# Kernel optimization log

Hardware: AMD Instinct MI355X
Metric: run time of the kernel (lower is better)

The kernel has to match this reference:

```python
import jax, jax.numpy as jnp
import numpy as np

V, D, L, H, S, B = 32000, 512, 4, 8, 2048, 2
HD = D // H
FF = 4 * D
EPS = 1e-5


def _ln(x, w, b):
    m = jnp.mean(x, axis=-1, keepdims=True)
    v = jnp.var(x, axis=-1, keepdims=True)
    return (x - m) / jnp.sqrt(v + EPS) * w + b


def setup_inputs() -> dict:
    key = jax.random.key(0)
    ks = jax.random.split(key, 32)
    rn = lambda k, shape, s=0.02: jax.random.normal(k, shape, jnp.float32) * s
    return {
        'x': jax.random.randint(ks[0], (B, S), 0, V),
        'tok_emb': rn(ks[1], (V, D)),
        'pos_emb': rn(ks[2], (S, D)),
        'qw': rn(ks[3], (L, D, D)), 'qb': rn(ks[4], (L, D)),
        'kw': rn(ks[5], (L, D, D)), 'kb': rn(ks[6], (L, D)),
        'vw': rn(ks[7], (L, D, D)), 'vb': rn(ks[8], (L, D)),
        'ow': rn(ks[9], (L, D, D)), 'ob': rn(ks[10], (L, D)),
        'qphase': rn(ks[11], (L, H), 0.1),
        'sp_phase': rn(ks[12], (L, D), 0.1),
        'n1w': jnp.ones((L, D), jnp.float32), 'n1b': jnp.zeros((L, D), jnp.float32),
        'n2w': jnp.ones((L, D), jnp.float32), 'n2b': jnp.zeros((L, D), jnp.float32),
        'f1w': rn(ks[13], (L, D, FF)), 'f1b': rn(ks[14], (L, FF)),
        'f2w': rn(ks[15], (L, FF, D)), 'f2b': rn(ks[16], (L, D)),
        'iw': rn(ks[17], (L, D, D)), 'ib': rn(ks[18], (L, D)),
        'gw': rn(ks[19], (L, D, D)), 'gb': rn(ks[20], (L, D)),
        'nw': jnp.ones((D,), jnp.float32), 'nb': jnp.zeros((D,), jnp.float32),
        'outw': rn(ks[21], (D, V)), 'outb': rn(ks[22], (V,)),
    }


def _forward(x, tok_emb, pos_emb, qw, qb, kw, kb, vw, vb, ow, ob, qphase, sp_phase,
             n1w, n1b, n2w, n2b, f1w, f1b, f2w, f2b, iw, ib, gw, gb, nw, nb, outw, outb):
    Bx, Sx = x.shape
    h = tok_emb[x] + pos_emb[:Sx][None, :, :]          # [B,S,D]
    mask = jnp.tril(jnp.ones((Sx, Sx), dtype=bool))    # causal
    scale = 1.0 / np.sqrt(HD).astype(np.float32)
    for l in range(L):
        # quantum attention with phase-modulated scores
        hn = _ln(h, n1w[l], n1b[l])
        q = (hn @ qw[l] + qb[l]).reshape(Bx, Sx, H, HD)
        k = (hn @ kw[l] + kb[l]).reshape(Bx, Sx, H, HD)
        v = (hn @ vw[l] + vb[l]).reshape(Bx, Sx, H, HD)
        scores = jnp.einsum('bqhd,bkhd->bhqk', q, k) * scale
        qi = jnp.cos(qphase[l][None, :, None, None] * scores)
        scores = scores * (1.0 + 0.1 * qi)
        scores = jnp.where(mask[None, None], scores, -jnp.inf)
        attn = jax.nn.softmax(scores, axis=-1)
        o = jnp.einsum('bhqk,bkhd->bqhd', attn, v).reshape(Bx, Sx, D)
        h = h + o @ ow[l] + ob[l]
        # superposition: x * cos(phase * x)
        h = h * jnp.cos(sp_phase[l] * h)
        # feed-forward (exact GELU, as torch default)
        hn2 = _ln(h, n2w[l], n2b[l])
        h = h + jax.nn.gelu(hn2 @ f1w[l] + f1b[l], approximate=False) @ f2w[l] + f2b[l]
        # interference gate
        g = jax.nn.sigmoid(h @ gw[l] + gb[l])
        h = (h @ iw[l] + ib[l]) * g + h * (1.0 - g)
    h = _ln(h, nw, nb)
    return h @ outw + outb                              # [B,S,V] logits


def reference(x, tok_emb, pos_emb, qw, qb, kw, kb, vw, vb, ow, ob, qphase, sp_phase,
              n1w, n1b, n2w, n2b, f1w, f1b, f2w, f2b, iw, ib, gw, gb, nw, nb, outw, outb):
    return _forward(x, tok_emb, pos_emb, qw, qb, kw, kb, vw, vb, ow, ob, qphase, sp_phase,
                    n1w, n1b, n2w, n2b, f1w, f1b, f2w, f2b, iw, ib, gw, gb, nw, nb, outw, outb)
```

## Files before the change

kernel.cpp:

```cpp
#include <hip/hip_runtime.h>
#include <math.h>

#define DIM 512
#define NH 8
#define HD 64
#define SEQ 2048
#define BATCH 2
#define NLAYER 4
#define FFD 2048
#define VOCAB 32000
#define ROWS (BATCH*SEQ)
#define QKV_LD 1536

typedef unsigned short u16;
typedef __attribute__((ext_vector_type(8))) short bfrag;
typedef __attribute__((ext_vector_type(4))) short sfrag4;
typedef __attribute__((ext_vector_type(4))) float facc;

__device__ __forceinline__ u16 f2bf(float f){
  unsigned u = __builtin_bit_cast(unsigned, f);
  u += 0x7fff + ((u>>16)&1);
  return (u16)(u>>16);
}

typedef __attribute__((address_space(3))) unsigned int lds_u32;
typedef const __attribute__((address_space(1))) unsigned int glob_u32;
__device__ __forceinline__ void gload16(const void* g, void* l){
  __builtin_amdgcn_global_load_lds((glob_u32*)g, (lds_u32*)l, 16, 0, 0);
}

template<int N> __device__ __forceinline__ void wait_vmcnt(){
  if constexpr (N==0)      asm volatile("s_waitcnt vmcnt(0)" ::: "memory");
  else if constexpr (N==3) asm volatile("s_waitcnt vmcnt(3)" ::: "memory");
  else if constexpr (N==4) asm volatile("s_waitcnt vmcnt(4)" ::: "memory");
  else if constexpr (N==6) asm volatile("s_waitcnt vmcnt(6)" ::: "memory");
  else if constexpr (N==8) asm volatile("s_waitcnt vmcnt(8)" ::: "memory");
  else static_assert(N==0, "unsupported vmcnt");
}

__global__ void transpose_w(const float* __restrict__ in, u16* __restrict__ out,
                            int K, int N, size_t zStride, int nOff, int imode){
  __shared__ float t[32][33];
  const int bz = blockIdx.z;
  const float* I = in + (size_t)bz*K*N;
  u16* O = out + (size_t)bz*zStride;
  const int n0 = blockIdx.x*32, k0 = blockIdx.y*32;
  #pragma unroll
  for (int i=0;i<4;i++){
    int k = k0 + threadIdx.y + 8*i;
    t[threadIdx.y+8*i][threadIdx.x] = I[(size_t)k*N + n0 + threadIdx.x];
  }
  __syncthreads();
  #pragma unroll
  for (int i=0;i<4;i++){
    int n = n0 + threadIdx.y + 8*i;
    int np = (imode==0) ? n : ((n>>4)*32 + (n&15) + (imode==2 ? 16 : 0));
    O[(size_t)(nOff+np)*K + k0 + threadIdx.x] = f2bf(t[threadIdx.x][threadIdx.y+8*i]);
  }
}

__global__ void concat3_k(const float* __restrict__ a, const float* __restrict__ b,
                          const float* __restrict__ c, float* __restrict__ o){
  int idx = blockIdx.x*256 + threadIdx.x;
  int l = idx/1536, r = idx%1536;
  float v = (r<512) ? a[l*512+r] : (r<1024 ? b[l*512+r-512] : c[l*512+r-1024]);
  o[idx] = v;
}
__global__ void concat2i_k(const float* __restrict__ ib, const float* __restrict__ gb,
                           float* __restrict__ o){
  int idx = blockIdx.x*256 + threadIdx.x;
  int l = idx>>10, cp = idx&1023;
  int bb = cp>>4, c = (bb>>1)*16 + (cp&15);
  o[idx] = (bb&1) ? gb[l*512+c] : ib[l*512+c];
}

__global__ void embed_k(const int* __restrict__ x, const float* __restrict__ tok,
                        const float* __restrict__ pos, float* __restrict__ h){
  int idx = blockIdx.x*256 + threadIdx.x;
  int row = idx >> 7;
  int d4  = idx & 127;
  int s   = row & (SEQ-1);
  int tkn = x[row];
  float4 tv = *(const float4*)(tok + (size_t)tkn*DIM + d4*4);
  float4 pv = *(const float4*)(pos + (size_t)s*DIM + d4*4);
  float4 r; r.x=tv.x+pv.x; r.y=tv.y+pv.y; r.z=tv.z+pv.z; r.w=tv.w+pv.w;
  *(float4*)(h + (size_t)row*DIM + d4*4) = r;
}

__global__ __launch_bounds__(256) void ln_k(const float* __restrict__ h,
    const float* __restrict__ w, const float* __restrict__ bsc,
    u16* __restrict__ out){
  const int wid = threadIdx.x>>6, lane = threadIdx.x&63;
  const int row = blockIdx.x*4 + wid;
  const float* r = h + (size_t)row*DIM + lane*8;
  float4 v0 = *(const float4*)r;
  float4 v1 = *(const float4*)(r+4);
  float s  = v0.x+v0.y+v0.z+v0.w + v1.x+v1.y+v1.z+v1.w;
  float ss = v0.x*v0.x+v0.y*v0.y+v0.z*v0.z+v0.w*v0.w
           + v1.x*v1.x+v1.y*v1.y+v1.z*v1.z+v1.w*v1.w;
  #pragma unroll
  for (int m=1;m<64;m<<=1){ s += __shfl_xor(s,m); ss += __shfl_xor(ss,m); }
  const float mean = s*(1.f/DIM);
  const float var  = ss*(1.f/DIM) - mean*mean;
  const float rsd  = rsqrtf(var + 1e-5f);
  float4 w0 = *(const float4*)(w + lane*8);
  float4 w1 = *(const float4*)(w + lane*8 + 4);
  float4 b0 = *(const float4*)(bsc + lane*8);
  float4 b1 = *(const float4*)(bsc + lane*8 + 4);
  bfrag pk;
  pk[0]=(short)f2bf((v0.x-mean)*rsd*w0.x+b0.x);
  pk[1]=(short)f2bf((v0.y-mean)*rsd*w0.y+b0.y);
  pk[2]=(short)f2bf((v0.z-mean)*rsd*w0.z+b0.z);
  pk[3]=(short)f2bf((v0.w-mean)*rsd*w0.w+b0.w);
  pk[4]=(short)f2bf((v1.x-mean)*rsd*w1.x+b1.x);
  pk[5]=(short)f2bf((v1.y-mean)*rsd*w1.y+b1.y);
  pk[6]=(short)f2bf((v1.z-mean)*rsd*w1.z+b1.z);
  pk[7]=(short)f2bf((v1.w-mean)*rsd*w1.w+b1.w);
  *(bfrag*)&out[(size_t)row*DIM + lane*8] = pk;
}

template<int BM,int BN,int BK,int WRN,int WCN,int DEPTH,int MODE>
__global__ __launch_bounds__(WRN*WCN*64, 2) void gemm_p(
    const u16* __restrict__ A, const u16* __restrict__ BT,
    const float* __restrict__ bias, const float* __restrict__ aux,
    float* __restrict__ Cf, u16* __restrict__ Cb, u16* __restrict__ vt,
    int M, int N, int K){
  constexpr int NTH = WRN*WCN*64;
  constexpr int FI  = BM/(16*WRN);
  constexpr int FJ  = BN/(16*WCN);
  constexpr int CPR = BK/8;
  constexpr int LA  = BM*CPR/NTH;
  constexpr int LB  = BN*CPR/NTH;
  constexpr int LPT = LA+LB;
  constexpr int NKK = BK/32;
  extern __shared__ __align__(16) u16 smem[];
  u16* lds_a = smem;
  u16* lds_b = smem + DEPTH*BM*BK;

  const int tid = threadIdx.x;
  const int wid = tid>>6, lane = tid&63;
  const int wr = wid / WCN, wc = wid % WCN;
  const int lr = lane&15, lg = lane>>4;
  const unsigned nwg = gridDim.x*gridDim.y;
  const unsigned lin = blockIdx.y*gridDim.x + blockIdx.x;
  const unsigned q = nwg >> 3;
  const unsigned sw = (lin & 7)*q + (lin >> 3);
  const int tm = sw % gridDim.x, tn = sw / gridDim.x;

  auto swzf = [](int row)->int{ return (BK==64) ? (row&7) : ((row>>1)&3); };

  auto stage = [&](int t, int buf){
    const int k0 = t*BK;
    #pragma unroll
    for (int i=0;i<LA;i++){
      int u = i*NTH + tid;
      int row = u/CPR, c = (u%CPR) ^ swzf(row);
      gload16(&A[(size_t)(tm*BM+row)*K + k0 + c*8], &lds_a[buf*BM*BK + u*8]);
    }
    #pragma unroll
    for (int i=0;i<LB;i++){
      int u = i*NTH + tid;
      int row = u/CPR, c = (u%CPR) ^ swzf(row);
      gload16(&BT[(size_t)(tn*BN+row)*K + k0 + c*8], &lds_b[buf*BN*BK + u*8]);
    }
  };

  facc acc[FI][FJ] = {};
  const int NT = K/BK;
  stage(0,0);
  if (NT>1) stage(1,1);
  if constexpr (DEPTH==3) { if (NT>2) stage(2,2); }
  for (int t=0;t<NT;t++){
    const int buf = t % DEPTH;
    const u16* la = &lds_a[buf*BM*BK];
    const u16* lb = &lds_b[buf*BN*BK];
    const int rem = NT-1-t;
    if constexpr (DEPTH==3){
      if (rem >= 2) wait_vmcnt<2*LPT>();
      else if (rem == 1) wait_vmcnt<LPT>();
      else wait_vmcnt<0>();
    } else {
      if (rem >= 1) wait_vmcnt<LPT>(); else wait_vmcnt<0>();
    }
    __builtin_amdgcn_s_barrier();
    __builtin_amdgcn_sched_barrier(0);
    bfrag af[FI], bf[FJ];
    #pragma unroll
    for (int i=0;i<FI;i++){
      int row = wr*(FI*16) + i*16 + lr;
      af[i] = *(const bfrag*)&la[row*BK + ((lg ^ swzf(row))*8)];
    }
    #pragma unroll
    for (int j=0;j<FJ;j++){
      int row = wc*(FJ*16) + j*16 + lr;
      bf[j] = *(const bfrag*)&lb[row*BK + ((lg ^ swzf(row))*8)];
    }
    if constexpr (NKK==1){
      asm volatile("s_waitcnt lgkmcnt(0)" ::: "memory");
      __builtin_amdgcn_sched_barrier(0);
      __builtin_amdgcn_s_barrier();
      __builtin_amdgcn_sched_barrier(0);
      if (t+DEPTH<NT) stage(t+DEPTH, buf);
      __builtin_amdgcn_s_setprio(1);
      #pragma unroll
      for (int i=0;i<FI;i++)
        #pragma unroll
        for (int j=0;j<FJ;j++)
          acc[i][j] = __builtin_amdgcn_mfma_f32_16x16x32_bf16(af[i], bf[j], acc[i][j],0,0,0);
      __builtin_amdgcn_s_setprio(0);
    } else {
      __builtin_amdgcn_s_setprio(1);
      #pragma unroll
      for (int i=0;i<FI;i++)
        #pragma unroll
        for (int j=0;j<FJ;j++)
          acc[i][j] = __builtin_amdgcn_mfma_f32_16x16x32_bf16(af[i], bf[j], acc[i][j],0,0,0);
      __builtin_amdgcn_s_setprio(0);
      bfrag af1[FI], bf1[FJ];
      #pragma unroll
      for (int i=0;i<FI;i++){
        int row = wr*(FI*16) + i*16 + lr;
        af1[i] = *(const bfrag*)&la[row*BK + (((4+lg) ^ swzf(row))*8)];
      }
      #pragma unroll
      for (int j=0;j<FJ;j++){
        int row = wc*(FJ*16) + j*16 + lr;
        bf1[j] = *(const bfrag*)&lb[row*BK + (((4+lg) ^ swzf(row))*8)];
      }
      asm volatile("s_waitcnt lgkmcnt(0)" ::: "memory");
      __builtin_amdgcn_sched_barrier(0);
      __builtin_amdgcn_s_barrier();
      __builtin_amdgcn_sched_barrier(0);
      if (t+DEPTH<NT) stage(t+DEPTH, buf);
      __builtin_amdgcn_s_setprio(1);
      #pragma unroll
      for (int i=0;i<FI;i++)
        #pragma unroll
        for (int j=0;j<FJ;j++)
          acc[i][j] = __builtin_amdgcn_mfma_f32_16x16x32_bf16(af1[i], bf1[j], acc[i][j],0,0,0);
      __builtin_amdgcn_s_setprio(0);
    }
  }

  if constexpr (MODE==5){
    #pragma unroll
    for (int i=0;i<FI;i++){
      #pragma unroll
      for (int j=0;j<FJ;j+=2){
        const int colp = tn*BN + wc*(FJ*16) + j*16;
        const int c = (colp>>5)*16 + lr;
        const float bi = bias[colp + lr];
        const float bg = bias[colp + 16 + lr];
        #pragma unroll
        for (int r=0;r<4;r++){
          const int row = tm*BM + wr*(FI*16) + i*16 + lg*4 + r;
          float vi = acc[i][j][r]   + bi;
          float vg = acc[i][j+1][r] + bg;
          float g  = 1.f/(1.f+__expf(-vg));
          const size_t o = (size_t)row*DIM + c;
          float hv = Cf[o];
          Cf[o] = vi*g + hv*(1.f-g);
        }
      }
    }
  } else if constexpr (MODE==7){
    #pragma unroll
    for (int i=0;i<FI;i++){
      #pragma unroll
      for (int j=0;j<FJ;j++){
        const int colblk = tn*BN + wc*(FJ*16) + j*16;
        const float bv = bias[colblk + lr];
        if (colblk < 1024){
          #pragma unroll
          for (int r=0;r<4;r++){
            const int row = tm*BM + wr*(FI*16) + i*16 + lg*4 + r;
            Cb[(size_t)row*N + colblk + lr] = f2bf(acc[i][j][r] + bv);
          }
        } else {
          const int c = colblk + lr - 1024;
          const int hh = c>>6, d = c&63;
          const int row0 = tm*BM + wr*(FI*16) + i*16 + lg*4;
          const int b = row0>>11, s0 = row0&2047;
          sfrag4 pk;
          #pragma unroll
          for (int r=0;r<4;r++) pk[r] = (short)f2bf(acc[i][j][r] + bv);
          *(sfrag4*)&vt[((size_t)((b*NH+hh)*HD + d))*SEQ + s0] = pk;
        }
      }
    }
  } else {
    #pragma unroll
    for (int i=0;i<FI;i++){
      #pragma unroll
      for (int j=0;j<FJ;j++){
        const int col = tn*BN + wc*(FJ*16) + j*16 + lr;
        const float bv = bias ? bias[col] : 0.f;
        #pragma unroll
        for (int r=0;r<4;r++){
          const int row = tm*BM + wr*(FI*16) + i*16 + lg*4 + r;
          float v = acc[i][j][r] + bv;
          const size_t o = (size_t)row*N + col;
          if      (MODE==0) Cf[o] = v;
          else if (MODE==3){ float g = 0.5f*v*(1.f+erff(v*0.70710678118f)); Cb[o] = f2bf(g); }
          else if (MODE==4){ float t = Cf[o] + v; t = t*__cosf(aux[col]*t); Cf[o] = t; }
          else if (MODE==6){ float t = Cf[o] + v; Cf[o] = t; Cb[o] = f2bf(t); }
        }
      }
    }
  }
}

__global__ __launch_bounds__(256) void attn_k(
    const u16* __restrict__ QKV, const u16* __restrict__ VT,
    const float* __restrict__ qphase, u16* __restrict__ O){
  __shared__ __align__(16) u16 lds_p[4][16*64];
  const int bx = blockIdx.x;
  const int qblk = (bx&1) ? (31 - (bx>>1)) : (bx>>1);
  const int hh = blockIdx.y, b = blockIdx.z;
  const int tid = threadIdx.x;
  const int wid = tid>>6, lane = tid&63;
  const int lr = lane&15, lg = lane>>4;
  const int qbase = qblk*64 + wid*16;
  const float ph = qphase[hh];
  const float scale = 0.125f;
  u16* pbuf = lds_p[wid];

  bfrag aq[2];
  #pragma unroll
  for (int st=0; st<2; st++)
    aq[st] = *(const bfrag*)&QKV[(size_t)(b*SEQ + qbase + lr)*QKV_LD + hh*HD + st*32 + lg*8];

  facc oacc[4] = {};
  float lrow[4] = {0.f,0.f,0.f,0.f};

  const int nkv = qblk + 1;
  for (int kt=0; kt<nkv; kt++){
    const int kv0 = kt*64;
    facc sc[4];
    #pragma unroll
    for (int j=0;j<4;j++){
      bfrag bk0 = *(const bfrag*)&QKV[(size_t)(b*SEQ + kv0 + j*16 + lr)*QKV_LD + 512 + hh*HD + lg*8];
      bfrag bk1 = *(const bfrag*)&QKV[(size_t)(b*SEQ + kv0 + j*16 + lr)*QKV_LD + 512 + hh*HD + 32 + lg*8];
      facc z = (facc){0.f,0.f,0.f,0.f};
      z     = __builtin_amdgcn_mfma_f32_16x16x32_bf16(aq[0], bk0, z, 0,0,0);
      sc[j] = __builtin_amdgcn_mfma_f32_16x16x32_bf16(aq[1], bk1, z, 0,0,0);
    }
    float pv[4][4];
    #pragma unroll
    for (int j=0;j<4;j++)
      #pragma unroll
      for (int r=0;r<4;r++){
        int srow = qbase + lg*4 + r;
        int scol = kv0 + j*16 + lr;
        float xv = sc[j][r]*scale;
        xv = xv*(1.f + 0.1f*__cosf(ph*xv));
        if (scol > srow) xv = -1e30f;
        pv[j][r] = __expf(xv);
      }
    #pragma unroll
    for (int r=0;r<4;r++){
      float rs = (pv[0][r]+pv[1][r]) + (pv[2][r]+pv[3][r]);
      rs += __shfl_xor(rs,1);
      rs += __shfl_xor(rs,2);
      rs += __shfl_xor(rs,4);
      rs += __shfl_xor(rs,8);
      lrow[r] += rs;
    }
    #pragma unroll
    for (int j=0;j<4;j++)
      #pragma unroll
      for (int r=0;r<4;r++){
        int prow = lg*4 + r;
        pbuf[prow*64 + ((j*16+lr) ^ ((prow&7)<<3))] = f2bf(pv[j][r]);
      }
    #pragma unroll
    for (int ks=0; ks<2; ks++){
      bfrag pa = *(const bfrag*)&pbuf[lr*64 + ((ks*32 + lg*8) ^ ((lr&7)<<3))];
      #pragma unroll
      for (int n=0;n<4;n++){
        bfrag vb = *(const bfrag*)&VT[((size_t)((b*NH + hh)*HD + n*16 + lr))*SEQ + kv0 + ks*32 + lg*8];
        oacc[n] = __builtin_amdgcn_mfma_f32_16x16x32_bf16(pa, vb, oacc[n], 0,0,0);
      }
    }
  }
  float rcp[4];
  #pragma unroll
  for (int r=0;r<4;r++) rcp[r] = 1.f/lrow[r];
  #pragma unroll
  for (int n=0;n<4;n++)
    #pragma unroll
    for (int r=0;r<4;r++){
      float val = oacc[n][r] * rcp[r];
      O[(size_t)(b*SEQ + qbase + lg*4 + r)*DIM + hh*HD + n*16 + lr] = f2bf(val);
    }
}

extern "C" void kernel_launch(void* const* d_in, const int* in_sizes, int n_in,
                              void* d_out, int out_size, void* d_ws, size_t ws_size,
                              hipStream_t stream){
  const int*   x        = (const int*)d_in[0];
  const float* tok_emb  = (const float*)d_in[1];
  const float* pos_emb  = (const float*)d_in[2];
  const float* qw = (const float*)d_in[3];  const float* qb = (const float*)d_in[4];
  const float* kw = (const float*)d_in[5];  const float* kb = (const float*)d_in[6];
  const float* vw = (const float*)d_in[7];  const float* vb = (const float*)d_in[8];
  const float* ow = (const float*)d_in[9];  const float* ob = (const float*)d_in[10];
  const float* qphase   = (const float*)d_in[11];
  const float* sp_phase = (const float*)d_in[12];
  const float* n1w = (const float*)d_in[13]; const float* n1b = (const float*)d_in[14];
  const float* n2w = (const float*)d_in[15]; const float* n2b = (const float*)d_in[16];
  const float* f1w = (const float*)d_in[17]; const float* f1b = (const float*)d_in[18];
  const float* f2w = (const float*)d_in[19]; const float* f2b = (const float*)d_in[20];
  const float* iw  = (const float*)d_in[21]; const float* ib  = (const float*)d_in[22];
  const float* gw  = (const float*)d_in[23]; const float* gb  = (const float*)d_in[24];
  const float* nw  = (const float*)d_in[25]; const float* nb  = (const float*)d_in[26];
  const float* outw= (const float*)d_in[27]; const float* outb= (const float*)d_in[28];
  float* out = (float*)d_out;

  char* base = (char*)d_ws;
  size_t off = 0;
  auto alloc = [&](size_t bytes)->void*{
    void* p = base + off; off += bytes; off = (off + 255) & ~(size_t)255; return p;
  };
  float* h    = (float*)alloc((size_t)ROWS*DIM*4);
  u16* hn     = (u16*)alloc((size_t)ROWS*DIM*2);
  u16* qkvB   = (u16*)alloc((size_t)ROWS*QKV_LD*2);
  u16* vTb    = (u16*)alloc((size_t)ROWS*DIM*2);
  u16* oB     = (u16*)alloc((size_t)ROWS*DIM*2);
  u16* hB     = (u16*)alloc((size_t)ROWS*DIM*2);
  u16* ffB    = (u16*)alloc((size_t)ROWS*FFD*2);
  u16* qkvT = (u16*)alloc((size_t)NLAYER*1536*DIM*2);
  u16* owT  = (u16*)alloc((size_t)NLAYER*DIM*DIM*2);
  u16* igT  = (u16*)alloc((size_t)NLAYER*1024*DIM*2);
  u16* f1T  = (u16*)alloc((size_t)NLAYER*DIM*FFD*2);
  u16* f2T  = (u16*)alloc((size_t)NLAYER*DIM*FFD*2);
  u16* outT = (u16*)alloc((size_t)VOCAB*DIM*2);
  float* qkvb = (float*)alloc((size_t)NLAYER*1536*4);
  float* igb  = (float*)alloc((size_t)NLAYER*1024*4);

  dim3 tb(32,8);
  transpose_w<<<dim3(DIM/32, DIM/32, NLAYER), tb, 0, stream>>>(qw, qkvT, DIM, DIM, (size_t)1536*DIM, 0, 0);
  transpose_w<<<dim3(DIM/32, DIM/32, NLAYER), tb, 0, stream>>>(kw, qkvT, DIM, DIM, (size_t)1536*DIM, 512, 0);
  transpose_w<<<dim3(DIM/32, DIM/32, NLAYER), tb, 0, stream>>>(vw, qkvT, DIM, DIM, (size_t)1536*DIM, 1024, 0);
  transpose_w<<<dim3(DIM/32, DIM/32, NLAYER), tb, 0, stream>>>(ow, owT, DIM, DIM, (size_t)DIM*DIM, 0, 0);
  transpose_w<<<dim3(DIM/32, DIM/32, NLAYER), tb, 0, stream>>>(iw, igT, DIM, DIM, (size_t)1024*DIM, 0, 1);
  transpose_w<<<dim3(DIM/32, DIM/32, NLAYER), tb, 0, stream>>>(gw, igT, DIM, DIM, (size_t)1024*DIM, 0, 2);
  transpose_w<<<dim3(FFD/32, DIM/32, NLAYER), tb, 0, stream>>>(f1w, f1T, DIM, FFD, (size_t)DIM*FFD, 0, 0);
  transpose_w<<<dim3(DIM/32, FFD/32, NLAYER), tb, 0, stream>>>(f2w, f2T, FFD, DIM, (size_t)DIM*FFD, 0, 0);
  transpose_w<<<dim3(VOCAB/32, DIM/32, 1),    tb, 0, stream>>>(outw, outT, DIM, VOCAB, 0, 0, 0);
  concat3_k<<<NLAYER*1536/256, 256, 0, stream>>>(qb, kb, vb, qkvb);
  concat2i_k<<<NLAYER*1024/256, 256, 0, stream>>>(ib, gb, igb);

  embed_k<<<ROWS*DIM/4/256, 256, 0, stream>>>(x, tok_emb, pos_emb, h);

  constexpr size_t SM_MID = 3*(128+128)*32*2;
  constexpr size_t SM_ROW = 3*(64+128)*32*2;
  constexpr size_t SM_BIG = 2*(256+256)*64*2;

  for (int l=0;l<NLAYER;l++){
    ln_k<<<ROWS/4, 256, 0, stream>>>(h, n1w + l*DIM, n1b + l*DIM, hn);
    gemm_p<128,128,32,2,2,3,7><<<dim3(ROWS/128, 1536/128), 256, SM_MID, stream>>>(
        hn, qkvT + (size_t)l*1536*DIM, qkvb + l*1536, nullptr, nullptr, qkvB, vTb, ROWS, 1536, DIM);
    attn_k<<<dim3(SEQ/64, NH, BATCH), 256, 0, stream>>>(qkvB, vTb, qphase + l*NH, oB);
    gemm_p<64,128,32,1,4,3,4><<<dim3(ROWS/64, DIM/128), 256, SM_ROW, stream>>>(
        oB, owT + (size_t)l*DIM*DIM, ob + l*DIM, sp_phase + l*DIM, h, nullptr, nullptr, ROWS, DIM, DIM);
    ln_k<<<ROWS/4, 256, 0, stream>>>(h, n2w + l*DIM, n2b + l*DIM, hn);
    gemm_p<128,128,32,2,2,3,3><<<dim3(ROWS/128, FFD/128), 256, SM_MID, stream>>>(
        hn, f1T + (size_t)l*DIM*FFD, f1b + l*FFD, nullptr, nullptr, ffB, nullptr, ROWS, FFD, DIM);
    gemm_p<64,128,32,1,4,3,6><<<dim3(ROWS/64, DIM/128), 256, SM_ROW, stream>>>(
        ffB, f2T + (size_t)l*DIM*FFD, f2b + l*DIM, nullptr, h, hB, nullptr, ROWS, DIM, FFD);
    gemm_p<128,128,32,2,2,3,5><<<dim3(ROWS/128, 1024/128), 256, SM_MID, stream>>>(
        hB, igT + (size_t)l*1024*DIM, igb + l*1024, nullptr, h, nullptr, nullptr, ROWS, 1024, DIM);
  }
  ln_k<<<ROWS/4, 256, 0, stream>>>(h, nw, nb, hn);
  gemm_p<256,256,64,2,4,2,0><<<dim3(ROWS/256, VOCAB/256), 512, SM_BIG, stream>>>(
      hn, outT, outb, nullptr, out, nullptr, nullptr, ROWS, VOCAB, DIM);
}
```

Measured before the change: 1.235 ms.

## Fold LayerNorm into GEMM epilogues via precomputed row statistics and weight folding

Removes the standalone LayerNorm kernels. The LN scale is folded into the transposed weights, and column sums (cs) and bias terms (cb) are precomputed, so each GEMM applies the mean/rstd correction in its epilogue. The producing epilogues (embed, MODE 4, MODE 5) now emit a bf16 copy of h plus per-tile partial sums and sums of squares, which the consuming GEMM reduces into the row mean and rstd. It also merges the weight transpose launches into one kernel and drops GEMM pipeline depth from 3 to 2. The costs are the numerically weaker one-pass variance computed from bf16-rounded activations, extra epilogue work and stores, and less latency hiding from the shallower pipeline.

```diff
diff --git a/kernel.cpp b/kernel.cpp
--- a/kernel.cpp
+++ b/kernel.cpp
@@ -38,34 +38,96 @@
   else static_assert(N==0, "unsupported vmcnt");
 }
 
-__global__ void transpose_w(const float* __restrict__ in, u16* __restrict__ out,
-                            int K, int N, size_t zStride, int nOff, int imode){
+__device__ __forceinline__ void do_transpose(
+    const float* __restrict__ I, u16* __restrict__ O,
+    int K, int N, int nx, int ky, const float* __restrict__ fw, int imode){
   __shared__ float t[32][33];
-  const int bz = blockIdx.z;
-  const float* I = in + (size_t)bz*K*N;
-  u16* O = out + (size_t)bz*zStride;
-  const int n0 = blockIdx.x*32, k0 = blockIdx.y*32;
+  const int n0 = nx*32, k0 = ky*32;
   #pragma unroll
   for (int i=0;i<4;i++){
     int k = k0 + threadIdx.y + 8*i;
     t[threadIdx.y+8*i][threadIdx.x] = I[(size_t)k*N + n0 + threadIdx.x];
   }
   __syncthreads();
+  const float wk = fw ? fw[k0+threadIdx.x] : 1.f;
   #pragma unroll
   for (int i=0;i<4;i++){
     int n = n0 + threadIdx.y + 8*i;
     int np = (imode==0) ? n : ((n>>4)*32 + (n&15) + (imode==2 ? 16 : 0));
-    O[(size_t)(nOff+np)*K + k0 + threadIdx.x] = f2bf(t[threadIdx.x][threadIdx.y+8*i]);
-  }
-}
-
-__global__ void concat3_k(const float* __restrict__ a, const float* __restrict__ b,
-                          const float* __restrict__ c, float* __restrict__ o){
+    O[(size_t)np*K + k0 + threadIdx.x] = f2bf(t[threadIdx.x][threadIdx.y+8*i] * wk);
+  }
+}
+
+__global__ void transpose_all(
+    const float* qw, const float* kw, const float* vw, const float* ow,
+    const float* iw, const float* gw, const float* f1w, const float* f2w,
+    const float* outw, const float* n1w, const float* n2w, const float* nw,
+    u16* qkvT, u16* owT, u16* igT, u16* f1T, u16* f2T, u16* outT){
+  int bid = blockIdx.x;
+  if (bid < 6144){
+    int job = bid >> 10, local = bid & 1023;
+    int l = local >> 8, rr = local & 255;
+    int nx = rr & 15, ky = rr >> 4;
+    const float* src; u16* dst; const float* fw = nullptr; int im = 0;
+    switch(job){
+      case 0: src=qw+(size_t)l*262144; dst=qkvT+(size_t)l*786432;        fw=n1w+l*512; break;
+      case 1: src=kw+(size_t)l*262144; dst=qkvT+(size_t)l*786432+262144; fw=n1w+l*512; break;
+      case 2: src=vw+(size_t)l*262144; dst=qkvT+(size_t)l*786432+524288; fw=n1w+l*512; break;
+      case 3: src=ow+(size_t)l*262144; dst=owT +(size_t)l*262144;        break;
+      case 4: src=iw+(size_t)l*262144; dst=igT +(size_t)l*524288; im=1;  break;
+      default:src=gw+(size_t)l*262144; dst=igT +(size_t)l*524288; im=2;  break;
+    }
+    do_transpose(src, dst, 512, 512, nx, ky, fw, im);
+  } else if (bid < 10240){
+    int local = bid - 6144;
+    int l = local >> 10, rr = local & 1023;
+    int nx = rr & 63, ky = rr >> 6;
+    do_transpose(f1w+(size_t)l*1048576, f1T+(size_t)l*1048576, 512, 2048, nx, ky, n2w+l*512, 0);
+  } else if (bid < 14336){
+    int local = bid - 10240;
+    int l = local >> 10, rr = local & 1023;
+    int nx = rr & 15, ky = rr >> 4;
+    do_transpose(f2w+(size_t)l*1048576, f2T+(size_t)l*1048576, 2048, 512, nx, ky, nullptr, 0);
+  } else {
+    int local = bid - 14336;
+    int nx = local % 1000, ky = local / 1000;
+    do_transpose(outw, outT, 512, 32000, nx, ky, nw, 0);
+  }
+}
+
+__global__ void foldvec_k(
+    const float* qw, const float* kw, const float* vw,
+    const float* qb, const float* kb, const float* vb,
+    const float* n1w, const float* n1b,
+    const float* f1w, const float* f1b, const float* n2w, const float* n2b,
+    const float* outw, const float* outb, const float* nw, const float* nb,
+    float* __restrict__ csB, float* __restrict__ cbB){
   int idx = blockIdx.x*256 + threadIdx.x;
-  int l = idx/1536, r = idx%1536;
-  float v = (r<512) ? a[l*512+r] : (r<1024 ? b[l*512+r-512] : c[l*512+r-1024]);
-  o[idx] = v;
-}
+  if (idx >= 46336) return;
+  const float* W; int stride; const float* wv; const float* bv; float biasv;
+  if (idx < 6144){
+    int l = idx/1536, c = idx%1536, sel = c>>9, c2 = c&511;
+    W = (sel==0?qw:sel==1?kw:vw) + (size_t)l*262144 + c2;
+    stride = 512; wv = n1w + l*512; bv = n1b + l*512;
+    biasv = (sel==0?qb:sel==1?kb:vb)[l*512+c2];
+  } else if (idx < 14336){
+    int t = idx-6144, l = t>>11, c = t&2047;
+    W = f1w + (size_t)l*1048576 + c;
+    stride = 2048; wv = n2w + l*512; bv = n2b + l*512;
+    biasv = f1b[l*2048+c];
+  } else {
+    int c = idx-14336;
+    W = outw + c; stride = 32000; wv = nw; bv = nb;
+    biasv = outb[c];
+  }
+  float cs = 0.f, cb = 0.f;
+  for (int k=0;k<512;k++){
+    float v = W[(size_t)k*stride];
+    cs += wv[k]*v; cb += bv[k]*v;
+  }
+  csB[idx] = cs; cbB[idx] = cb + biasv;
+}
+
 __global__ void concat2i_k(const float* __restrict__ ib, const float* __restrict__ gb,
                            float* __restrict__ o){
   int idx = blockIdx.x*256 + threadIdx.x;
@@ -74,57 +136,40 @@
   o[idx] = (bb&1) ? gb[l*512+c] : ib[l*512+c];
 }
 
-__global__ void embed_k(const int* __restrict__ x, const float* __restrict__ tok,
-                        const float* __restrict__ pos, float* __restrict__ h){
-  int idx = blockIdx.x*256 + threadIdx.x;
-  int row = idx >> 7;
-  int d4  = idx & 127;
-  int s   = row & (SEQ-1);
-  int tkn = x[row];
-  float4 tv = *(const float4*)(tok + (size_t)tkn*DIM + d4*4);
-  float4 pv = *(const float4*)(pos + (size_t)s*DIM + d4*4);
-  float4 r; r.x=tv.x+pv.x; r.y=tv.y+pv.y; r.z=tv.z+pv.z; r.w=tv.w+pv.w;
-  *(float4*)(h + (size_t)row*DIM + d4*4) = r;
-}
-
-__global__ __launch_bounds__(256) void ln_k(const float* __restrict__ h,
-    const float* __restrict__ w, const float* __restrict__ bsc,
-    u16* __restrict__ out){
+__global__ __launch_bounds__(256) void embed_k(const int* __restrict__ x,
+    const float* __restrict__ tok, const float* __restrict__ pos,
+    float* __restrict__ h, u16* __restrict__ hA, float* __restrict__ pst){
   const int wid = threadIdx.x>>6, lane = threadIdx.x&63;
   const int row = blockIdx.x*4 + wid;
-  const float* r = h + (size_t)row*DIM + lane*8;
-  float4 v0 = *(const float4*)r;
-  float4 v1 = *(const float4*)(r+4);
-  float s  = v0.x+v0.y+v0.z+v0.w + v1.x+v1.y+v1.z+v1.w;
-  float ss = v0.x*v0.x+v0.y*v0.y+v0.z*v0.z+v0.w*v0.w
-           + v1.x*v1.x+v1.y*v1.y+v1.z*v1.z+v1.w*v1.w;
+  const int s   = row & (SEQ-1);
+  const int tkn = x[row];
+  const float* tp = tok + (size_t)tkn*DIM + lane*8;
+  const float* pp = pos + (size_t)s*DIM + lane*8;
+  float4 t0 = *(const float4*)tp,     t1 = *(const float4*)(tp+4);
+  float4 p0 = *(const float4*)pp,     p1 = *(const float4*)(pp+4);
+  float4 a; a.x=t0.x+p0.x; a.y=t0.y+p0.y; a.z=t0.z+p0.z; a.w=t0.w+p0.w;
+  float4 b; b.x=t1.x+p1.x; b.y=t1.y+p1.y; b.z=t1.z+p1.z; b.w=t1.w+p1.w;
+  float* hp = h + (size_t)row*DIM + lane*8;
+  *(float4*)hp = a; *(float4*)(hp+4) = b;
+  bfrag pk;
+  pk[0]=(short)f2bf(a.x); pk[1]=(short)f2bf(a.y); pk[2]=(short)f2bf(a.z); pk[3]=(short)f2bf(a.w);
+  pk[4]=(short)f2bf(b.x); pk[5]=(short)f2bf(b.y); pk[6]=(short)f2bf(b.z); pk[7]=(short)f2bf(b.w);
+  *(bfrag*)&hA[(size_t)row*DIM + lane*8] = pk;
+  float S  = a.x+a.y+a.z+a.w + b.x+b.y+b.z+b.w;
+  float SS = a.x*a.x+a.y*a.y+a.z*a.z+a.w*a.w + b.x*b.x+b.y*b.y+b.z*b.z+b.w*b.w;
   #pragma unroll
-  for (int m=1;m<64;m<<=1){ s += __shfl_xor(s,m); ss += __shfl_xor(ss,m); }
-  const float mean = s*(1.f/DIM);
-  const float var  = ss*(1.f/DIM) - mean*mean;
-  const float rsd  = rsqrtf(var + 1e-5f);
-  float4 w0 = *(const float4*)(w + lane*8);
-  float4 w1 = *(const float4*)(w + lane*8 + 4);
-  float4 b0 = *(const float4*)(bsc + lane*8);
-  float4 b1 = *(const float4*)(bsc + lane*8 + 4);
-  bfrag pk;
-  pk[0]=(short)f2bf((v0.x-mean)*rsd*w0.x+b0.x);
-  pk[1]=(short)f2bf((v0.y-mean)*rsd*w0.y+b0.y);
-  pk[2]=(short)f2bf((v0.z-mean)*rsd*w0.z+b0.z);
-  pk[3]=(short)f2bf((v0.w-mean)*rsd*w0.w+b0.w);
-  pk[4]=(short)f2bf((v1.x-mean)*rsd*w1.x+b1.x);
-  pk[5]=(short)f2bf((v1.y-mean)*rsd*w1.y+b1.y);
-  pk[6]=(short)f2bf((v1.z-mean)*rsd*w1.z+b1.z);
-  pk[7]=(short)f2bf((v1.w-mean)*rsd*w1.w+b1.w);
-  *(bfrag*)&out[(size_t)row*DIM + lane*8] = pk;
-}
-
-template<int BM,int BN,int BK,int WRN,int WCN,int DEPTH,int MODE>
+  for (int m=1;m<64;m<<=1){ S += __shfl_xor(S,m); SS += __shfl_xor(SS,m); }
+  if (lane==0){ pst[(size_t)row*32+0]=S; pst[(size_t)row*32+1]=SS; }
+}
+
+template<int BM,int BN,int BK,int WRN,int WCN,int DEPTH,int MODE,int FOLD>
 __global__ __launch_bounds__(WRN*WCN*64, 2) void gemm_p(
     const u16* __restrict__ A, const u16* __restrict__ BT,
     const float* __restrict__ bias, const float* __restrict__ aux,
     float* __restrict__ Cf, u16* __restrict__ Cb, u16* __restrict__ vt,
-    int M, int N, int K){
+    const float* __restrict__ cs, const float* __restrict__ cb,
+    const float* __restrict__ pst_in, float* __restrict__ pst_out,
+    u16* __restrict__ hA, int M, int N, int K, int pstP){
   constexpr int NTH = WRN*WCN*64;
   constexpr int FI  = BM/(16*WRN);
   constexpr int FJ  = BN/(16*WCN);
@@ -133,9 +178,11 @@
   constexpr int LB  = BN*CPR/NTH;
   constexpr int LPT = LA+LB;
   constexpr int NKK = BK/32;
+  constexpr int STE = DEPTH*(BM+BN)*BK;
   extern __shared__ __align__(16) u16 smem[];
   u16* lds_a = smem;
   u16* lds_b = smem + DEPTH*BM*BK;
+  float* stf = (float*)(smem + STE);
 
   const int tid = threadIdx.x;
   const int wid = tid>>6, lane = tid&63;
@@ -168,8 +215,22 @@
   facc acc[FI][FJ] = {};
   const int NT = K/BK;
   stage(0,0);
+  __builtin_amdgcn_sched_barrier(0);
+  if constexpr (FOLD){
+    if (tid < BM){
+      const float* p = pst_in + (size_t)(tm*BM+tid)*32;
+      float S=0.f, SS=0.f;
+      for (int q2=0;q2<pstP;q2++){ S += p[2*q2]; SS += p[2*q2+1]; }
+      float mu = S*(1.f/512.f);
+      float var = SS*(1.f/512.f) - mu*mu;
+      stf[tid*2]   = mu;
+      stf[tid*2+1] = rsqrtf(var + 1e-5f);
+    }
+    __builtin_amdgcn_sched_barrier(0);
+  }
   if (NT>1) stage(1,1);
   if constexpr (DEPTH==3) { if (NT>2) stage(2,2); }
+
   for (int t=0;t<NT;t++){
     const int buf = t % DEPTH;
     const u16* la = &lds_a[buf*BM*BK];
@@ -242,7 +303,17 @@
     }
   }
 
+  auto fold = [&](float av, int i, int r, int col)->float{
+    if constexpr (FOLD){
+      const int lrow = wr*(FI*16) + i*16 + lg*4 + r;
+      return stf[lrow*2+1]*(av - stf[lrow*2]*cs[col]) + cb[col];
+    } else {
+      return av + (bias ? bias[col] : 0.f);
+    }
+  };
+
   if constexpr (MODE==5){
+    float sA[FI][4] = {}, sQ[FI][4] = {};
     #pragma unroll
     for (int i=0;i<FI;i++){
       #pragma unroll
@@ -259,51 +330,108 @@
           float g  = 1.f/(1.f+__expf(-vg));
           const size_t o = (size_t)row*DIM + c;
           float hv = Cf[o];
-          Cf[o] = vi*g + hv*(1.f-g);
+          float tvv = vi*g + hv*(1.f-g);
+          Cf[o] = tvv;
+          hA[(size_t)row*DIM + c] = f2bf(tvv);
+          sA[i][r] += tvv; sQ[i][r] += tvv*tvv;
         }
       }
     }
+    #pragma unroll
+    for (int i=0;i<FI;i++)
+      #pragma unroll
+      for (int r=0;r<4;r++){
+        float s = sA[i][r], qq = sQ[i][r];
+        s += __shfl_xor(s,1); qq += __shfl_xor(qq,1);
+        s += __shfl_xor(s,2); qq += __shfl_xor(qq,2);
+        s += __shfl_xor(s,4); qq += __shfl_xor(qq,4);
+        s += __shfl_xor(s,8); qq += __shfl_xor(qq,8);
+        if (lr==0){
+          const int row = tm*BM + wr*(FI*16) + i*16 + lg*4 + r;
+          const int slot = tn*2 + wc;
+          pst_out[(size_t)row*32 + slot*2]   = s;
+          pst_out[(size_t)row*32 + slot*2+1] = qq;
+        }
+      }
   } else if constexpr (MODE==7){
     #pragma unroll
     for (int i=0;i<FI;i++){
       #pragma unroll
       for (int j=0;j<FJ;j++){
         const int colblk = tn*BN + wc*(FJ*16) + j*16;
-        const float bv = bias[colblk + lr];
+        const int col = colblk + lr;
+        float tv[4];
+        #pragma unroll
+        for (int r=0;r<4;r++) tv[r] = fold(acc[i][j][r], i, r, col);
         if (colblk < 1024){
           #pragma unroll
           for (int r=0;r<4;r++){
             const int row = tm*BM + wr*(FI*16) + i*16 + lg*4 + r;
-            Cb[(size_t)row*N + colblk + lr] = f2bf(acc[i][j][r] + bv);
+            Cb[(size_t)row*N + col] = f2bf(tv[r]);
           }
         } else {
-          const int c = colblk + lr - 1024;
+          const int c = col - 1024;
           const int hh = c>>6, d = c&63;
           const int row0 = tm*BM + wr*(FI*16) + i*16 + lg*4;
           const int b = row0>>11, s0 = row0&2047;
           sfrag4 pk;
           #pragma unroll
-          for (int r=0;r<4;r++) pk[r] = (short)f2bf(acc[i][j][r] + bv);
+          for (int r=0;r<4;r++) pk[r] = (short)f2bf(tv[r]);
           *(sfrag4*)&vt[((size_t)((b*NH+hh)*HD + d))*SEQ + s0] = pk;
         }
       }
     }
-  } else {
+  } else if constexpr (MODE==4){
+    float sA[FI][4] = {}, sQ[FI][4] = {};
     #pragma unroll
     for (int i=0;i<FI;i++){
       #pragma unroll
       for (int j=0;j<FJ;j++){
         const int col = tn*BN + wc*(FJ*16) + j*16 + lr;
-        const float bv = bias ? bias[col] : 0.f;
+        const float av = aux[col];
         #pragma unroll
         for (int r=0;r<4;r++){
           const int row = tm*BM + wr*(FI*16) + i*16 + lg*4 + r;
-          float v = acc[i][j][r] + bv;
+          float v = fold(acc[i][j][r], i, r, col);
+          const size_t o = (size_t)row*N + col;
+          float tvv = Cf[o] + v;
+          tvv = tvv*__cosf(av*tvv);
+          Cf[o] = tvv;
+          hA[(size_t)row*DIM + col] = f2bf(tvv);
+          sA[i][r] += tvv; sQ[i][r] += tvv*tvv;
+        }
+      }
+    }
+    #pragma unroll
+    for (int i=0;i<FI;i++)
+      #pragma unroll
+      for (int r=0;r<4;r++){
+        float s = sA[i][r], qq = sQ[i][r];
+        s += __shfl_xor(s,1); qq += __shfl_xor(qq,1);
+        s += __shfl_xor(s,2); qq += __shfl_xor(qq,2);
+        s += __shfl_xor(s,4); qq += __shfl_xor(qq,4);
+        s += __shfl_xor(s,8); qq += __shfl_xor(qq,8);
+        if (lr==0){
+          const int row = tm*BM + wr*(FI*16) + i*16 + lg*4 + r;
+          const int slot = tn*4 + wc;
+          pst_out[(size_t)row*32 + slot*2]   = s;
+          pst_out[(size_t)row*32 + slot*2+1] = qq;
+        }
+      }
+  } else {
+    #pragma unroll
+    for (int i=0;i<FI;i++){
+      #pragma unroll
+      for (int j=0;j<FJ;j++){
+        const int col = tn*BN + wc*(FJ*16) + j*16 + lr;
+        #pragma unroll
+        for (int r=0;r<4;r++){
+          const int row = tm*BM + wr*(FI*16) + i*16 + lg*4 + r;
+          float v = fold(acc[i][j][r], i, r, col);
           const size_t o = (size_t)row*N + col;
           if      (MODE==0) Cf[o] = v;
           else if (MODE==3){ float g = 0.5f*v*(1.f+erff(v*0.70710678118f)); Cb[o] = f2bf(g); }
-          else if (MODE==4){ float t = Cf[o] + v; t = t*__cosf(aux[col]*t); Cf[o] = t; }
-          else if (MODE==6){ float t = Cf[o] + v; Cf[o] = t; Cb[o] = f2bf(t); }
+          else if (MODE==6){ float tvv = Cf[o] + v; Cf[o] = tvv; Cb[o] = f2bf(tvv); }
         }
       }
     }
@@ -423,56 +551,61 @@
     void* p = base + off; off += bytes; off = (off + 255) & ~(size_t)255; return p;
   };
   float* h    = (float*)alloc((size_t)ROWS*DIM*4);
-  u16* hn     = (u16*)alloc((size_t)ROWS*DIM*2);
+  u16* hAb    = (u16*)alloc((size_t)ROWS*DIM*2);
+  u16* hB     = (u16*)alloc((size_t)ROWS*DIM*2);
   u16* qkvB   = (u16*)alloc((size_t)ROWS*QKV_LD*2);
   u16* vTb    = (u16*)alloc((size_t)ROWS*DIM*2);
   u16* oB     = (u16*)alloc((size_t)ROWS*DIM*2);
-  u16* hB     = (u16*)alloc((size_t)ROWS*DIM*2);
   u16* ffB    = (u16*)alloc((size_t)ROWS*FFD*2);
+  float* pst  = (float*)alloc((size_t)ROWS*32*4);
   u16* qkvT = (u16*)alloc((size_t)NLAYER*1536*DIM*2);
   u16* owT  = (u16*)alloc((size_t)NLAYER*DIM*DIM*2);
   u16* igT  = (u16*)alloc((size_t)NLAYER*1024*DIM*2);
   u16* f1T  = (u16*)alloc((size_t)NLAYER*DIM*FFD*2);
   u16* f2T  = (u16*)alloc((size_t)NLAYER*DIM*FFD*2);
   u16* outT = (u16*)alloc((size_t)VOCAB*DIM*2);
-  float* qkvb = (float*)alloc((size_t)NLAYER*1536*4);
-  float* igb  = (float*)alloc((size_t)NLAYER*1024*4);
+  float* csB = (float*)alloc((size_t)46336*4);
+  float* cbB = (float*)alloc((size_t)46336*4);
+  float* igb = (float*)alloc((size_t)NLAYER*1024*4);
 
   dim3 tb(32,8);
-  transpose_w<<<dim3(DIM/32, DIM/32, NLAYER), tb, 0, stream>>>(qw, qkvT, DIM, DIM, (size_t)1536*DIM, 0, 0);
-  transpose_w<<<dim3(DIM/32, DIM/32, NLAYER), tb, 0, stream>>>(kw, qkvT, DIM, DIM, (size_t)1536*DIM, 512, 0);
-  transpose_w<<<dim3(DIM/32, DIM/32, NLAYER), tb, 0, stream>>>(vw, qkvT, DIM, DIM, (size_t)1536*DIM, 1024, 0);
-  transpose_w<<<dim3(DIM/32, DIM/32, NLAYER), tb, 0, stream>>>(ow, owT, DIM, DIM, (size_t)DIM*DIM, 0, 0);
-  transpose_w<<<dim3(DIM/32, DIM/32, NLAYER), tb, 0, stream>>>(iw, igT, DIM, DIM, (size_t)1024*DIM, 0, 1);
-  transpose_w<<<dim3(DIM/32, DIM/32, NLAYER), tb, 0, stream>>>(gw, igT, DIM, DIM, (size_t)1024*DIM, 0, 2);
-  transpose_w<<<dim3(FFD/32, DIM/32, NLAYER), tb, 0, stream>>>(f1w, f1T, DIM, FFD, (size_t)DIM*FFD, 0, 0);
-  transpose_w<<<dim3(DIM/32, FFD/32, NLAYER), tb, 0, stream>>>(f2w, f2T, FFD, DIM, (size_t)DIM*FFD, 0, 0);
-  transpose_w<<<dim3(VOCAB/32, DIM/32, 1),    tb, 0, stream>>>(outw, outT, DIM, VOCAB, 0, 0, 0);
-  concat3_k<<<NLAYER*1536/256, 256, 0, stream>>>(qb, kb, vb, qkvb);
+  transpose_all<<<30336, tb, 0, stream>>>(qw,kw,vw,ow,iw,gw,f1w,f2w,outw,
+                                          n1w,n2w,nw, qkvT,owT,igT,f1T,f2T,outT);
+  foldvec_k<<<182, 256, 0, stream>>>(qw,kw,vw,qb,kb,vb,n1w,n1b,
+                                     f1w,f1b,n2w,n2b,outw,outb,nw,nb, csB,cbB);
   concat2i_k<<<NLAYER*1024/256, 256, 0, stream>>>(ib, gb, igb);
-
-  embed_k<<<ROWS*DIM/4/256, 256, 0, stream>>>(x, tok_emb, pos_emb, h);
-
-  constexpr size_t SM_MID = 3*(128+128)*32*2;
-  constexpr size_t SM_ROW = 3*(64+128)*32*2;
-  constexpr size_t SM_BIG = 2*(256+256)*64*2;
+  embed_k<<<ROWS/4, 256, 0, stream>>>(x, tok_emb, pos_emb, h, hAb, pst);
+
+  constexpr size_t SM_MID  = 2*(128+128)*32*2;
+  constexpr size_t SM_MIDF = SM_MID + 128*2*4;
+  constexpr size_t SM_ROW  = 2*(64+128)*32*2;
+  constexpr size_t SM_BIG  = 2*(256+256)*64*2 + 256*2*4;
 
   for (int l=0;l<NLAYER;l++){
-    ln_k<<<ROWS/4, 256, 0, stream>>>(h, n1w + l*DIM, n1b + l*DIM, hn);
-    gemm_p<128,128,32,2,2,3,7><<<dim3(ROWS/128, 1536/128), 256, SM_MID, stream>>>(
-        hn, qkvT + (size_t)l*1536*DIM, qkvb + l*1536, nullptr, nullptr, qkvB, vTb, ROWS, 1536, DIM);
+    gemm_p<128,128,32,2,2,2,7,1><<<dim3(ROWS/128, 1536/128), 256, SM_MIDF, stream>>>(
+        hAb, qkvT + (size_t)l*1536*DIM, nullptr, nullptr,
+        nullptr, qkvB, vTb, csB + l*1536, cbB + l*1536,
+        pst, nullptr, nullptr, ROWS, 1536, DIM, l==0 ? 1 : 16);
     attn_k<<<dim3(SEQ/64, NH, BATCH), 256, 0, stream>>>(qkvB, vTb, qphase + l*NH, oB);
-    gemm_p<64,128,32,1,4,3,4><<<dim3(ROWS/64, DIM/128), 256, SM_ROW, stream>>>(
-        oB, owT + (size_t)l*DIM*DIM, ob + l*DIM, sp_phase + l*DIM, h, nullptr, nullptr, ROWS, DIM, DIM);
-    ln_k<<<ROWS/4, 256, 0, stream>>>(h, n2w + l*DIM, n2b + l*DIM, hn);
-    gemm_p<128,128,32,2,2,3,3><<<dim3(ROWS/128, FFD/128), 256, SM_MID, stream>>>(
-        hn, f1T + (size_t)l*DIM*FFD, f1b + l*FFD, nullptr, nullptr, ffB, nullptr, ROWS, FFD, DIM);
-    gemm_p<64,128,32,1,4,3,6><<<dim3(ROWS/64, DIM/128), 256, SM_ROW, stream>>>(
-        ffB, f2T + (size_t)l*DIM*FFD, f2b + l*DIM, nullptr, h, hB, nullptr, ROWS, DIM, FFD);
-    gemm_p<128,128,32,2,2,3,5><<<dim3(ROWS/128, 1024/128), 256, SM_MID, stream>>>(
-        hB, igT + (size_t)l*1024*DIM, igb + l*1024, nullptr, h, nullptr, nullptr, ROWS, 1024, DIM);
-  }
-  ln_k<<<ROWS/4, 256, 0, stream>>>(h, nw, nb, hn);
-  gemm_p<256,256,64,2,4,2,0><<<dim3(ROWS/256, VOCAB/256), 512, SM_BIG, stream>>>(
-      hn, outT, outb, nullptr, out, nullptr, nullptr, ROWS, VOCAB, DIM);
-}
+    gemm_p<64,128,32,1,4,2,4,0><<<dim3(ROWS/64, DIM/128), 256, SM_ROW, stream>>>(
+        oB, owT + (size_t)l*DIM*DIM, ob + l*DIM, sp_phase + l*DIM,
+        h, nullptr, nullptr, nullptr, nullptr,
+        nullptr, pst, hAb, ROWS, DIM, DIM, 0);
+    gemm_p<128,128,32,2,2,2,3,1><<<dim3(ROWS/128, FFD/128), 256, SM_MIDF, stream>>>(
+        hAb, f1T + (size_t)l*DIM*FFD, nullptr, nullptr,
+        nullptr, ffB, nullptr, csB + 6144 + l*2048, cbB + 6144 + l*2048,
+        pst, nullptr, nullptr, ROWS, FFD, DIM, 16);
+    gemm_p<64,128,32,1,4,2,6,0><<<dim3(ROWS/64, DIM/128), 256, SM_ROW, stream>>>(
+        ffB, f2T + (size_t)l*DIM*FFD, f2b + l*DIM, nullptr,
+        h, hB, nullptr, nullptr, nullptr,
+        nullptr, nullptr, nullptr, ROWS, DIM, FFD, 0);
+    gemm_p<128,128,32,2,2,2,5,0><<<dim3(ROWS/128, 1024/128), 256, SM_MID, stream>>>(
+        hB, igT + (size_t)l*1024*DIM, igb + l*1024, nullptr,
+        h, nullptr, nullptr, nullptr, nullptr,
+        nullptr, pst, hAb, ROWS, 1024, DIM, 0);
+  }
+  gemm_p<256,256,64,2,4,2,0,1><<<dim3(ROWS/256, VOCAB/256), 512, SM_BIG, stream>>>(
+      hAb, outT, nullptr, nullptr,
+      out, nullptr, nullptr, csB + 14336, cbB + 14336,
+      pst, nullptr, nullptr, ROWS, VOCAB, DIM, 16);
+}
```

Result: slower. 1.374 ms (+11.3%).
